# Performance work log

Hardware: AMD Instinct MI355X
Metric: run time of the kernel (lower is better)

The kernel has to match this reference:

```python
import jax, jax.numpy as jnp
import numpy as np

EPS = 0.1          # noise magnitude
N_LAYERS = 3
LAYER_CL = 1
USER_NUM = 100000
ITEM_NUM = 50000
NUM_ENTITIES = 100000  # padding entity id == NUM_ENTITIES
E_PER_ITEM = 16
NNZ = 4500000
EMB = 64
ALPHA = 0.2        # leaky-relu slope in GAT


def setup_inputs() -> dict:
    key = jax.random.key(0)
    ks = jax.random.split(key, 12)
    inp = {}
    inp["user_emb"] = jax.random.normal(ks[0], (USER_NUM, EMB), jnp.float32) * 0.1
    inp["item_emb"] = jax.random.normal(ks[1], (ITEM_NUM, EMB), jnp.float32) * 0.1
    inp["entity_table"] = jax.random.normal(ks[2], (NUM_ENTITIES + 1, EMB), jnp.float32) * 0.1
    inp["relation_table"] = jax.random.normal(ks[3], (21, EMB), jnp.float32) * 0.1
    inp["fc_w"] = jax.random.normal(ks[4], (2 * EMB, EMB), jnp.float32) * (1.0 / np.sqrt(2 * EMB))
    inp["fc_b"] = jnp.zeros((EMB,), jnp.float32)
    inp["adj_rows"] = jax.random.randint(ks[5], (NNZ,), 0, USER_NUM + ITEM_NUM, jnp.int32)
    inp["adj_cols"] = jax.random.randint(ks[6], (NNZ,), 0, USER_NUM + ITEM_NUM, jnp.int32)
    # scale values like a degree-normalized adjacency so repeated spmm stays bounded
    inp["adj_vals"] = jax.random.uniform(ks[7], (NNZ,), jnp.float32) * (1.0 / 30.0)
    inp["users_noise"] = jax.random.uniform(ks[8], (N_LAYERS, USER_NUM, EMB), jnp.float32)
    inp["item_entities"] = jax.random.randint(ks[9], (ITEM_NUM, E_PER_ITEM), 0, NUM_ENTITIES + 1, jnp.int32)
    inp["item_relations"] = jax.random.randint(ks[10], (ITEM_NUM, E_PER_ITEM), 0, 20, jnp.int32)
    return inp


def _spmm(rows, cols, vals, x, n):
    # sparse (n x n) @ x via gather + segment_sum
    return jax.ops.segment_sum(vals[:, None] * x[cols], rows, num_segments=n)


def _gat_forward_relation(item_embs, entity_embs, relation_embs, mask, fc_w, fc_b):
    # item_embs [N,d], entity_embs [N,E,d], relation_embs [N,E,d], mask [N,E]
    N, E, d = entity_embs.shape
    Wh = jnp.broadcast_to(item_embs[:, None, :], (N, E, d))
    a_input = jnp.concatenate([Wh, entity_embs], axis=-1)            # [N,E,2d]
    e_pre = jnp.einsum('nek,kd->ned', a_input, fc_w) + fc_b          # fc(a_input)
    e = jax.nn.leaky_relu(jnp.sum(e_pre * relation_embs, axis=-1), ALPHA)  # [N,E]
    att = jnp.where(mask > 0, e, jnp.float32(-9e15))
    att = jax.nn.softmax(att, axis=1)
    agg = jnp.einsum('ne,ned->nd', att, entity_embs)
    return agg + item_embs


def _l2_normalize(x):
    # matches F.normalize(x, dim=-1) with eps=1e-12
    n = jnp.sqrt(jnp.sum(x * x, axis=-1, keepdims=True))
    return x / jnp.maximum(n, 1e-12)


def reference(user_emb, item_emb, entity_table, relation_table, fc_w, fc_b,
              adj_rows, adj_cols, adj_vals, users_noise,
              item_entities, item_relations):
    n_nodes = USER_NUM + ITEM_NUM
    # KG-based item embedding (deterministic across layers; gat has dropout=0)
    entity_embs = entity_table[item_entities]        # [I,E,d]
    relation_embs = relation_table[item_relations]   # [I,E,d]
    padding_mask = (item_entities != NUM_ENTITIES).astype(jnp.float32)
    items_emb2 = jax.nn.sigmoid(
        _gat_forward_relation(item_emb, entity_embs, relation_embs, padding_mask, fc_w, fc_b))

    ego = jnp.concatenate([user_emb, item_emb], axis=0)
    all_embeddings = []
    all_embeddings_cl = ego
    for k in range(N_LAYERS):
        ego = _spmm(adj_rows, adj_cols, adj_vals, ego, n_nodes)
        random_noise = jnp.concatenate([users_noise[k], items_emb2], axis=0)
        ego = ego + jnp.sign(ego) * _l2_normalize(random_noise) * EPS
        all_embeddings.append(ego)
        if k == LAYER_CL - 1:
            all_embeddings_cl = ego
    final = jnp.mean(jnp.stack(all_embeddings, axis=1), axis=1)
    user_all, item_all = final[:USER_NUM], final[USER_NUM:]
    user_cl, item_cl = all_embeddings_cl[:USER_NUM], all_embeddings_cl[USER_NUM:]
    return (user_all, item_all, user_cl, item_cl)
```

## Files before the change

kernel.cpp:

```cpp
#include <hip/hip_runtime.h>
#include <math.h>

#define EMBD   64
#define USERS  100000
#define ITEMS  50000
#define NODES  150000
#define NNZ_C  4500000
#define NENT   100000
#define EPER   16
#define NBLK_SCAN 586

#define NBKT   512
#define BROWS  293
#define NCHK   2048
#define CHSZ   2198
#define HN     (NBKT * NCHK)
#define HBLK   (HN / 256)

__device__ __forceinline__ float eigen_expf(float x) {
    x = fminf(fmaxf(x, -87.33654785156250f), 88.72283935546875f);
    float m = floorf(__fmaf_rn(x, 1.44269504088896341f, 0.5f));
    float r = __fsub_rn(x, __fmul_rn(m, 0.693359375f));
    r = __fsub_rn(r, __fmul_rn(m, -2.12194440e-4f));
    float z = __fmul_rn(r, r);
    float y = 1.9875691500e-4f;
    y = __fmaf_rn(y, r, 1.3981999507e-3f);
    y = __fmaf_rn(y, r, 8.3334519073e-3f);
    y = __fmaf_rn(y, r, 4.1665795894e-2f);
    y = __fmaf_rn(y, r, 1.6666665459e-1f);
    y = __fmaf_rn(y, r, 5.0000001201e-1f);
    y = __fmaf_rn(y, z, r);
    y = __fadd_rn(y, 1.0f);
    int mi = (int)m;
    return __int_as_float(__float_as_int(y) + (mi << 23));
}

__device__ __forceinline__ float eigen_tanhf(float x) {
    float ax = fabsf(x);
    float x2 = __fmul_rn(x, x);
    float p = -2.76076847742355e-16f;
    p = __fmaf_rn(p, x2, 2.00018790482477e-13f);
    p = __fmaf_rn(p, x2, -8.60467152213735e-11f);
    p = __fmaf_rn(p, x2, 5.12229709037114e-08f);
    p = __fmaf_rn(p, x2, 1.48572235717979e-05f);
    p = __fmaf_rn(p, x2, 6.37261928875436e-04f);
    p = __fmaf_rn(p, x2, 4.89352455891786e-03f);
    p = __fmul_rn(x, p);
    float q = 1.19825839466702e-06f;
    q = __fmaf_rn(q, x2, 1.18534705686654e-04f);
    q = __fmaf_rn(q, x2, 2.26843463243900e-03f);
    q = __fmaf_rn(q, x2, 4.89352518554385e-03f);
    float r = __fdiv_rn(p, q);
    return (ax < 4.0e-4f) ? x : r;
}

__device__ __forceinline__ float wave_sum64(float x) {
    float v = __fadd_rn(x, __shfl_xor(x, 16));
    v = __fadd_rn(v, __shfl_xor(v, 32));
    v = __fadd_rn(v, __shfl_xor(v, 8));
    v = __fadd_rn(v, __shfl_xor(v, 4));
    v = __fadd_rn(v, __shfl_xor(v, 2));
    v = __fadd_rn(v, __shfl_xor(v, 1));
    return v;
}

__device__ __forceinline__ float rdlane(float v, int l) {
    return __int_as_float(__builtin_amdgcn_readlane(__float_as_int(v), l));
}

__device__ __forceinline__ unsigned long long match_mask10(int key) {
    unsigned long long m = ~0ull;
    #pragma unroll
    for (int bit = 0; bit < 10; ++bit) {
        unsigned long long bb = __ballot((key >> bit) & 1);
        m &= ((key >> bit) & 1) ? bb : ~bb;
    }
    return m;
}

__global__ void scan1_kernel(const int* __restrict__ cnt, int* __restrict__ bsum) {
    __shared__ int s[256];
    int i = blockIdx.x * 256 + threadIdx.x;
    int v = (i < NODES) ? cnt[i] : 0;
    s[threadIdx.x] = v; __syncthreads();
    for (int o = 128; o; o >>= 1) {
        if (threadIdx.x < o) s[threadIdx.x] += s[threadIdx.x + o];
        __syncthreads();
    }
    if (threadIdx.x == 0) bsum[blockIdx.x] = s[0];
}

__global__ void scan2_kernel(int* __restrict__ bsum, int nblk) {
    if (blockIdx.x == 0 && threadIdx.x == 0) {
        int acc = 0;
        for (int b = 0; b < nblk; ++b) { int t = bsum[b]; bsum[b] = acc; acc += t; }
    }
}

__global__ void scan3_kernel(const int* __restrict__ cnt, const int* __restrict__ bsum,
                             int* __restrict__ rowptr) {
    __shared__ int s[256];
    int tid = threadIdx.x;
    int i = blockIdx.x * 256 + tid;
    int v = (i < NODES) ? cnt[i] : 0;
    s[tid] = v; __syncthreads();
    for (int o = 1; o < 256; o <<= 1) {
        int t = (tid >= o) ? s[tid - o] : 0;
        __syncthreads();
        s[tid] += t;
        __syncthreads();
    }
    if (i < NODES) rowptr[i] = bsum[blockIdx.x] + s[tid] - v;
}

__global__ __launch_bounds__(64) void hist_kernel(const int* __restrict__ rows,
                                                  int* __restrict__ H,
                                                  int* __restrict__ cnt) {
    __shared__ int h[NBKT];
    int lane = threadIdx.x;
    int w = blockIdx.x;
    for (int b = lane; b < NBKT; b += 64) h[b] = 0;
    __syncthreads();
    int start = w * CHSZ;
    int end = min(start + CHSZ, NNZ_C);
    for (int i = start + lane; i < end; i += 64) {
        int r = rows[i];
        atomicAdd(&h[r / BROWS], 1);
        atomicAdd(&cnt[r], 1);
    }
    __syncthreads();
    for (int b = lane; b < NBKT; b += 64) H[b * NCHK + w] = h[b];
}

__global__ void gscanA_kernel(const int* __restrict__ in, int* __restrict__ part) {
    __shared__ int s[256];
    int i = blockIdx.x * 256 + threadIdx.x;
    s[threadIdx.x] = in[i]; __syncthreads();
    for (int o = 128; o; o >>= 1) {
        if (threadIdx.x < o) s[threadIdx.x] += s[threadIdx.x + o];
        __syncthreads();
    }
    if (threadIdx.x == 0) part[blockIdx.x] = s[0];
}

__global__ void gscanC_kernel(const int* __restrict__ in, const int* __restrict__ part,
                              int* __restrict__ outp) {
    __shared__ int s[256];
    int tid = threadIdx.x;
    int i = blockIdx.x * 256 + tid;
    int v = in[i];
    s[tid] = v; __syncthreads();
    for (int o = 1; o < 256; o <<= 1) {
        int t = (tid >= o) ? s[tid - o] : 0;
        __syncthreads();
        s[tid] += t;
        __syncthreads();
    }
    outp[i] = part[blockIdx.x] + s[tid] - v;
}

__global__ __launch_bounds__(64) void scatter1_kernel(const int* __restrict__ rows,
                                                      const int* __restrict__ P,
                                                      int* __restrict__ bids) {
    __shared__ int curL[NBKT];
    __shared__ int tmpB[NBKT];
    int lane = threadIdx.x;
    int w = blockIdx.x;
    for (int b = lane; b < NBKT; b += 64) curL[b] = P[b * NCHK + w];
    __syncthreads();
    int start = w * CHSZ;
    int end = min(start + CHSZ, NNZ_C);
    for (int i = start; i < end; i += 64) {
        int e = i + lane;
        bool ok = (e < end);
        int b = ok ? (rows[e] / BROWS) : 0;
        int key = ok ? b : (NBKT + lane);
        unsigned long long m = match_mask10(key);
        int rank = __popcll(m & ((1ull << lane) - 1ull));
        int cntk = __popcll(m);
        if (ok && rank == 0) {
            int base = curL[b];
            curL[b] = base + cntk;
            tmpB[b] = base;
        }
        __syncthreads();
        if (ok) bids[tmpB[b] + rank] = e;
        __syncthreads();
    }
}

__global__ __launch_bounds__(64) void place_kernel(const int* __restrict__ rows,
                                                   const int* __restrict__ cols,
                                                   const float* __restrict__ vals,
                                                   const int* __restrict__ bids,
                                                   const int* __restrict__ P,
                                                   const int* __restrict__ rowp,
                                                   int2* __restrict__ pairs) {
    __shared__ int curR[BROWS];
    __shared__ int tmpB[BROWS];
    int lane = threadIdx.x;
    int b0 = blockIdx.x;
    for (int j = lane; j < BROWS; j += 64) curR[j] = 0;
    __syncthreads();
    int bs = P[b0 * NCHK];
    int be = (b0 == NBKT - 1) ? NNZ_C : P[(b0 + 1) * NCHK];
    for (int i = bs; i < be; i += 64) {
        int idx = i + lane;
        bool ok = (idx < be);
        int e = ok ? bids[idx] : 0;
        int r = ok ? rows[e] : 0;
        int rl = r - b0 * BROWS;
        int key = ok ? rl : (NBKT + lane);
        unsigned long long m = match_mask10(key);
        int rank = __popcll(m & ((1ull << lane) - 1ull));
        int cntk = __popcll(m);
        if (ok && rank == 0) {
            int base = curR[rl];
            curR[rl] = base + cntk;
            tmpB[rl] = base;
        }
        __syncthreads();
        if (ok) {
            int slot = rowp[r] + tmpB[rl] + rank;
            pairs[slot] = make_int2(cols[e], __float_as_int(vals[e]));
        }
        __syncthreads();
    }
}

#define NB 8
__global__ __launch_bounds__(256) void spmm_layer_kernel(
        const int*   __restrict__ rowptr,
        const int*   __restrict__ cnt,
        const int2*  __restrict__ pairs,
        const float* __restrict__ x,
        float*       __restrict__ y,
        const float* __restrict__ noise_k,
        const float* __restrict__ nitems,
        float*       __restrict__ out,
        int k) {
    int lane = threadIdx.x & 63;
    int r0 = (blockIdx.x * blockDim.x + threadIdx.x) >> 6;
    if (r0 >= NODES) return;
    int r = __builtin_amdgcn_readfirstlane(r0);
    int s = rowptr[r], n = cnt[r];
    const int2* p2 = pairs + s;

    float acc = 0.f;
    int i = 0;
    if (n >= NB) {
        float v[NB], g[NB];
        #pragma unroll
        for (int j = 0; j < NB; ++j) {
            int2 t = p2[j];
            v[j] = __int_as_float(t.y);
            g[j] = x[(size_t)t.x * EMBD + lane];
        }
        for (i = NB; i + NB <= n; i += NB) {
            float v2[NB], g2[NB];
            #pragma unroll
            for (int j = 0; j < NB; ++j) {
                int2 t = p2[i + j];
                v2[j] = __int_as_float(t.y);
                g2[j] = x[(size_t)t.x * EMBD + lane];
            }
            #pragma unroll
            for (int j = 0; j < NB; ++j)
                acc = __fadd_rn(acc, __fmul_rn(v[j], g[j]));
            #pragma unroll
            for (int j = 0; j < NB; ++j) { v[j] = v2[j]; g[j] = g2[j]; }
        }
        #pragma unroll
        for (int j = 0; j < NB; ++j)
            acc = __fadd_rn(acc, __fmul_rn(v[j], g[j]));
    }
    for (; i < n; ++i) {
        int2 t = p2[i];
        acc = __fadd_rn(acc, __fmul_rn(__int_as_float(t.y),
                                       x[(size_t)t.x * EMBD + lane]));
    }

    size_t idx = (size_t)r * EMBD + lane;
    float yv = acc;
    bool isu = (r < USERS);
    float v = isu ? noise_k[idx] : 0.f;
    float ss = wave_sum64(__fmul_rn(v, v));

    float nn;
    if (isu) nn = __fdiv_rn(v, fmaxf(__fsqrt_rn(ss), 1e-12f));
    else     nn = nitems[(size_t)(r - USERS) * EMBD + lane];

    float sg  = (yv > 0.f) ? 1.f : ((yv < 0.f) ? -1.f : 0.f);
    float ego = __fadd_rn(yv, __fmul_rn(__fmul_rn(sg, nn), 0.1f));

    y[idx] = ego;

    const size_t CL_OFF = (size_t)NODES * EMBD;
    if (k == 0) {
        out[idx]          = ego;
        out[CL_OFF + idx] = ego;
    } else if (k == 1) {
        out[idx] = __fadd_rn(out[idx], ego);
    } else {
        out[idx] = __fdiv_rn(__fadd_rn(out[idx], ego), 3.0f);
    }
}

__global__ __launch_bounds__(512) void gat_kernel(
        const float* __restrict__ item_emb,
        const float* __restrict__ ent_table,
        const float* __restrict__ fc_w,
        const float* __restrict__ fc_b,
        const float* __restrict__ rel_table,
        const int*   __restrict__ item_ents,
        const int*   __restrict__ item_rels,
        float*       __restrict__ nitems) {
    __shared__ float Wsh[128 * 64];
    int tid = threadIdx.x;
    for (int i = tid; i < 128 * 64; i += 512) Wsh[i] = fc_w[i];
    __syncthreads();

    int w = tid >> 6, lane = tid & 63;
    int n = __builtin_amdgcn_readfirstlane(blockIdx.x * 8 + w);
    const float* qrow = item_emb + (size_t)n * EMBD;
    float q  = qrow[lane];
    float bv = fc_b[lane];

    float accI = 0.f;
    #pragma unroll 1
    for (int kb = 0; kb < 16; ++kb) {
        float4 qv = *(const float4*)(qrow + kb * 4);
        accI = __fmaf_rn(qv.x, Wsh[(kb * 4 + 0) * 64 + lane], accI);
        accI = __fmaf_rn(qv.y, Wsh[(kb * 4 + 1) * 64 + lane], accI);
        accI = __fmaf_rn(qv.z, Wsh[(kb * 4 + 2) * 64 + lane], accI);
        accI = __fmaf_rn(qv.w, Wsh[(kb * 4 + 3) * 64 + lane], accI);
    }

    int eid[EPER];
    const float* er[EPER];
    float ev[EPER];
    #pragma unroll
    for (int e = 0; e < EPER; ++e) {
        eid[e] = __builtin_amdgcn_readfirstlane(item_ents[n * EPER + e]);
        er[e]  = ent_table + (size_t)eid[e] * EMBD;
        ev[e]  = er[e][lane];
    }

    float acc[EPER];
    #pragma unroll
    for (int e = 0; e < EPER; ++e) acc[e] = accI;
    #pragma unroll 1
    for (int kb = 0; kb < 16; ++kb) {
        float4 sv[10];
        #pragma unroll
        for (int eo = 0; eo < 10; ++eo)
            sv[eo] = *(const float4*)(er[6 + eo] + kb * 4);
        float wv0 = Wsh[(64 + kb * 4 + 0) * 64 + lane];
        float wv1 = Wsh[(64 + kb * 4 + 1) * 64 + lane];
        float wv2 = Wsh[(64 + kb * 4 + 2) * 64 + lane];
        float wv3 = Wsh[(64 + kb * 4 + 3) * 64 + lane];
        int k0 = kb * 4;
        #pragma unroll
        for (int eo = 0; eo < 6; ++eo) {
            acc[eo] = __fmaf_rn(rdlane(ev[eo], k0 + 0), wv0, acc[eo]);
            acc[eo] = __fmaf_rn(rdlane(ev[eo], k0 + 1), wv1, acc[eo]);
            acc[eo] = __fmaf_rn(rdlane(ev[eo], k0 + 2), wv2, acc[eo]);
            acc[eo] = __fmaf_rn(rdlane(ev[eo], k0 + 3), wv3, acc[eo]);
        }
        #pragma unroll
        for (int eo = 0; eo < 10; ++eo)
            acc[6 + eo] = __fmaf_rn(sv[eo].x, wv0, acc[6 + eo]);
        #pragma unroll
        for (int eo = 0; eo < 10; ++eo)
            acc[6 + eo] = __fmaf_rn(sv[eo].y, wv1, acc[6 + eo]);
        #pragma unroll
        for (int eo = 0; eo < 10; ++eo)
            acc[6 + eo] = __fmaf_rn(sv[eo].z, wv2, acc[6 + eo]);
        #pragma unroll
        for (int eo = 0; eo < 10; ++eo)
            acc[6 + eo] = __fmaf_rn(sv[eo].w, wv3, acc[6 + eo]);
    }

    float s16[EPER];
    #pragma unroll
    for (int e = 0; e < EPER; ++e) {
        int rid = item_rels[n * EPER + e];
        float pe   = __fadd_rn(acc[e], bv);
        float prod = __fmul_rn(pe, rel_table[rid * EMBD + lane]);
        float esum = wave_sum64(prod);
        float sc = (esum >= 0.f) ? esum : __fmul_rn(0.2f, esum);
        s16[e] = (eid[e] != NENT) ? sc : -9.0e15f;
    }

    float m = s16[0];
    #pragma unroll
    for (int e = 1; e < EPER; ++e) m = fmaxf(m, s16[e]);
    float a16[EPER];
    #pragma unroll
    for (int e = 0; e < EPER; ++e) a16[e] = eigen_expf(__fsub_rn(s16[e], m));
    float s8[8];
    #pragma unroll
    for (int j = 0; j < 8; ++j) s8[j] = __fadd_rn(a16[j], a16[j + 8]);
    float t40 = __fadd_rn(s8[0], s8[4]);
    float t41 = __fadd_rn(s8[1], s8[5]);
    float t42 = __fadd_rn(s8[2], s8[6]);
    float t43 = __fadd_rn(s8[3], s8[7]);
    float z = __fadd_rn(__fadd_rn(t40, t42), __fadd_rn(t41, t43));

    float agg = 0.f;
    #pragma unroll
    for (int e = 0; e < EPER; ++e)
        agg = __fmaf_rn(__fdiv_rn(a16[e], z), ev[e], agg);

    float o = __fadd_rn(agg, q);
    float t = eigen_tanhf(__fmul_rn(0.5f, o));
    float sig = __fmaf_rn(0.5f, t, 0.5f);

    float ss = wave_sum64(__fmul_rn(sig, sig));
    float nrm = fmaxf(__fsqrt_rn(ss), 1e-12f);
    nitems[(size_t)n * EMBD + lane] = __fdiv_rn(sig, nrm);
}

extern "C" void kernel_launch(void* const* d_in, const int* in_sizes, int n_in,
                              void* d_out, int out_size, void* d_ws, size_t ws_size,
                              hipStream_t stream) {
    const float* user_emb   = (const float*)d_in[0];
    const float* item_emb   = (const float*)d_in[1];
    const float* ent_table  = (const float*)d_in[2];
    const float* rel_table  = (const float*)d_in[3];
    const float* fc_w       = (const float*)d_in[4];
    const float* fc_b       = (const float*)d_in[5];
    const int*   adj_rows   = (const int*)d_in[6];
    const int*   adj_cols   = (const int*)d_in[7];
    const float* adj_vals   = (const float*)d_in[8];
    const float* users_noise= (const float*)d_in[9];
    const int*   item_ents  = (const int*)d_in[10];
    const int*   item_rels  = (const int*)d_in[11];

    const size_t NE = (size_t)NODES * EMBD;
    char* base = (char*)d_ws;
    size_t off = 0;
    float*  B0    = (float*)(base + off); off += NE * 4;
    float*  B1    = (float*)(base + off); off += NE * 4;
    float*  NIT   = (float*)(base + off); off += (size_t)ITEMS * EMBD * 4;
    int*    cnt   = (int*)(base + off);   off += 150016 * 4;
    int*    rowp  = (int*)(base + off);   off += 150016 * 4;
    int*    bsum  = (int*)(base + off);   off += 1024 * 4;
    int*    H     = (int*)(base + off);   off += (size_t)HN * 4;
    int*    gb    = (int*)(base + off);   off += (size_t)HBLK * 4;
    int*    g2    = (int*)(base + off);   off += 64 * 4;
    int*    gbE   = (int*)(base + off);   off += (size_t)HBLK * 4;
    int*    P     = (int*)(base + off);   off += (size_t)HN * 4;
    int*    bids  = (int*)(base + off);   off += (size_t)NNZ_C * 4;
    off = (off + 7) & ~(size_t)7;
    int2*   pairs = (int2*)(base + off);  off += (size_t)NNZ_C * 8;
    float*  out   = (float*)d_out;

    hipMemsetAsync(cnt, 0, 150016 * 4, stream);
    hist_kernel<<<NCHK, 64, 0, stream>>>(adj_rows, H, cnt);

    scan1_kernel<<<NBLK_SCAN, 256, 0, stream>>>(cnt, bsum);
    scan2_kernel<<<1, 64, 0, stream>>>(bsum, NBLK_SCAN);
    scan3_kernel<<<NBLK_SCAN, 256, 0, stream>>>(cnt, bsum, rowp);

    gscanA_kernel<<<HBLK, 256, 0, stream>>>(H, gb);
    gscanA_kernel<<<HBLK / 256, 256, 0, stream>>>(gb, g2);
    scan2_kernel<<<1, 64, 0, stream>>>(g2, HBLK / 256);
    gscanC_kernel<<<HBLK / 256, 256, 0, stream>>>(gb, g2, gbE);
    gscanC_kernel<<<HBLK, 256, 0, stream>>>(H, gbE, P);

    scatter1_kernel<<<NCHK, 64, 0, stream>>>(adj_rows, P, bids);
    place_kernel<<<NBKT, 64, 0, stream>>>(adj_rows, adj_cols, adj_vals,
                                          bids, P, rowp, pairs);

    hipMemcpyAsync(B0, user_emb, (size_t)USERS * EMBD * 4, hipMemcpyDeviceToDevice, stream);
    hipMemcpyAsync(B0 + (size_t)USERS * EMBD, item_emb, (size_t)ITEMS * EMBD * 4,
                   hipMemcpyDeviceToDevice, stream);

    gat_kernel<<<ITEMS / 8, 512, 0, stream>>>(item_emb, ent_table, fc_w, fc_b,
                                              rel_table, item_ents, item_rels, NIT);

    for (int k = 0; k < 3; ++k) {
        float* X = (k & 1) ? B1 : B0;
        float* Y = (k & 1) ? B0 : B1;
        spmm_layer_kernel<<<(NODES + 3) / 4, 256, 0, stream>>>(
            rowp, cnt, pairs, X, Y,
            users_noise + (size_t)k * USERS * EMBD, NIT, out, k);
    }
}
```

Baseline: 1.349 ms.

## Schedule SpMM rows in descending degree order via counting sort

Adds a degree histogram, a serial reverse scan, and an atomic scatter that build a row permutation sorted by nonzero count, largest first. The SpMM kernel then maps each wavefront to a permuted row, so heavy rows start early and load balance across waves improves. The cost is three extra small kernels, including a single-thread scan over 1024 bins. Rows also become scattered in memory order, which may hurt locality of row-indexed accesses such as noise, output and rowptr reads.

```diff
diff --git a/kernel.cpp b/kernel.cpp
--- a/kernel.cpp
+++ b/kernel.cpp
@@ -16,6 +16,7 @@
 #define CHSZ   2198
 #define HN     (NBKT * NCHK)
 #define HBLK   (HN / 256)
+#define DMAX   1024
 
 __device__ __forceinline__ float eigen_expf(float x) {
     x = fminf(fmaxf(x, -87.33654785156250f), 88.72283935546875f);
@@ -228,10 +229,33 @@
     }
 }
 
+__global__ void dhist_kernel(const int* __restrict__ cnt, int* __restrict__ dh) {
+    int r = blockIdx.x * 256 + threadIdx.x;
+    if (r < NODES) atomicAdd(&dh[min(cnt[r], DMAX - 1)], 1);
+}
+
+__global__ void dscan_kernel(int* __restrict__ dh) {
+    if (blockIdx.x == 0 && threadIdx.x == 0) {
+        int acc = 0;
+        for (int d = DMAX - 1; d >= 0; --d) { int t = dh[d]; dh[d] = acc; acc += t; }
+    }
+}
+
+__global__ void dscatter_kernel(const int* __restrict__ cnt, int* __restrict__ dh,
+                                int* __restrict__ rord) {
+    int r = blockIdx.x * 256 + threadIdx.x;
+    if (r < NODES) {
+        int d = min(cnt[r], DMAX - 1);
+        int slot = atomicAdd(&dh[d], 1);
+        rord[slot] = r;
+    }
+}
+
 #define NB 8
 __global__ __launch_bounds__(256) void spmm_layer_kernel(
         const int*   __restrict__ rowptr,
         const int*   __restrict__ cnt,
+        const int*   __restrict__ rord,
         const int2*  __restrict__ pairs,
         const float* __restrict__ x,
         float*       __restrict__ y,
@@ -242,7 +266,7 @@
     int lane = threadIdx.x & 63;
     int r0 = (blockIdx.x * blockDim.x + threadIdx.x) >> 6;
     if (r0 >= NODES) return;
-    int r = __builtin_amdgcn_readfirstlane(r0);
+    int r = __builtin_amdgcn_readfirstlane(rord[r0]);
     int s = rowptr[r], n = cnt[r];
     const int2* p2 = pairs + s;
 
@@ -445,7 +469,9 @@
     float*  NIT   = (float*)(base + off); off += (size_t)ITEMS * EMBD * 4;
     int*    cnt   = (int*)(base + off);   off += 150016 * 4;
     int*    rowp  = (int*)(base + off);   off += 150016 * 4;
+    int*    rord  = (int*)(base + off);   off += 150016 * 4;
     int*    bsum  = (int*)(base + off);   off += 1024 * 4;
+    int*    dh    = (int*)(base + off);   off += DMAX * 4;
     int*    H     = (int*)(base + off);   off += (size_t)HN * 4;
     int*    gb    = (int*)(base + off);   off += (size_t)HBLK * 4;
     int*    g2    = (int*)(base + off);   off += 64 * 4;
@@ -457,11 +483,16 @@
     float*  out   = (float*)d_out;
 
     hipMemsetAsync(cnt, 0, 150016 * 4, stream);
+    hipMemsetAsync(dh, 0, DMAX * 4, stream);
     hist_kernel<<<NCHK, 64, 0, stream>>>(adj_rows, H, cnt);
 
     scan1_kernel<<<NBLK_SCAN, 256, 0, stream>>>(cnt, bsum);
     scan2_kernel<<<1, 64, 0, stream>>>(bsum, NBLK_SCAN);
     scan3_kernel<<<NBLK_SCAN, 256, 0, stream>>>(cnt, bsum, rowp);
+
+    dhist_kernel<<<NBLK_SCAN, 256, 0, stream>>>(cnt, dh);
+    dscan_kernel<<<1, 64, 0, stream>>>(dh);
+    dscatter_kernel<<<NBLK_SCAN, 256, 0, stream>>>(cnt, dh, rord);
 
     gscanA_kernel<<<HBLK, 256, 0, stream>>>(H, gb);
     gscanA_kernel<<<HBLK / 256, 256, 0, stream>>>(gb, g2);
@@ -484,7 +515,7 @@
         float* X = (k & 1) ? B1 : B0;
         float* Y = (k & 1) ? B0 : B1;
         spmm_layer_kernel<<<(NODES + 3) / 4, 256, 0, stream>>>(
-            rowp, cnt, pairs, X, Y,
+            rowp, cnt, rord, pairs, X, Y,
             users_noise + (size_t)k * USERS * EMBD, NIT, out, k);
     }
 }
```

After: 2.055 ms. 52.3% more time.
